# Kernel tuning notes

Measured on AMD Instinct MI355X. Metric: run time of the kernel, lower is better.

Reference implementation:

```python
import jax, jax.numpy as jnp
import numpy as np

NU, NI, NB, D = 100000, 50000, 20000, 64
E_UI, E_UB, E_BI = 1_000_000, 600_000, 400_000
BATCH = 2048
NUM_LAYERS = 2
C_TEMP = 0.25


def _sym_laplacian(src, dst, n_src_offset, n_total):
    # bipartite graph made symmetric: edges (u, off+v) and (off+v, u), val 1.0
    row = np.concatenate([src, n_src_offset + dst])
    col = np.concatenate([n_src_offset + dst, src])
    deg = np.bincount(row, minlength=n_total).astype(np.float64)
    val = 1.0 / ((np.sqrt(deg[row]) + 1e-8) * (np.sqrt(deg[col]) + 1e-8))
    return row.astype(np.int32), col.astype(np.int32), val.astype(np.float32)


def setup_inputs() -> dict:
    rng = np.random.default_rng(0)
    ui_u = rng.integers(0, NU, E_UI)
    ui_i = rng.integers(0, NI, E_UI)
    ub_u = rng.integers(0, NU, E_UB)
    ub_b = rng.integers(0, NB, E_UB)
    bi_b = rng.integers(0, NB, E_BI)
    bi_i = rng.integers(0, NI, E_BI)

    il_row, il_col, il_val = _sym_laplacian(ui_u, ui_i, NU, NU + NI)
    bl_row, bl_col, bl_val = _sym_laplacian(ub_u, ub_b, NU, NU + NB)
    deg_b = np.bincount(bi_b, minlength=NB).astype(np.float64)
    agg_val = (1.0 / (deg_b + 1e-8))[bi_b].astype(np.float32)

    key = jax.random.key(0)
    k1, k2, k3 = jax.random.split(key, 3)
    std = 0.05  # xavier-ish init scale
    return {
        "users_feature": jax.random.normal(k1, (NU, D), jnp.float32) * std,
        "items_feature": jax.random.normal(k2, (NI, D), jnp.float32) * std,
        "bundles_feature": jax.random.normal(k3, (NB, D), jnp.float32) * std,
        "il_row": jnp.asarray(il_row), "il_col": jnp.asarray(il_col), "il_val": jnp.asarray(il_val),
        "bl_row": jnp.asarray(bl_row), "bl_col": jnp.asarray(bl_col), "bl_val": jnp.asarray(bl_val),
        "agg_row": jnp.asarray(bi_b.astype(np.int32)), "agg_col": jnp.asarray(bi_i.astype(np.int32)),
        "agg_val": jnp.asarray(agg_val),
        "users": jnp.asarray(rng.integers(0, NU, BATCH).astype(np.int32)),
        "bundles": jnp.asarray(rng.integers(0, NB, (BATCH, 2)).astype(np.int32)),
    }


def _spmm(row, col, val, feat, n):
    # COO SpMM: out[r] += val * feat[c]   (gather + segment-sum, memory bound)
    return jax.ops.segment_sum(val[:, None] * feat[col], row, num_segments=n)


def _one_propagate(row, col, val, A, B):
    f = jnp.concatenate([A, B], axis=0)
    n = f.shape[0]
    acc = f
    for i in range(NUM_LAYERS):
        f = _spmm(row, col, val, f, n) / (i + 2)
        nrm = jnp.maximum(jnp.linalg.norm(f, axis=1, keepdims=True), 1e-12)
        acc = acc + f / nrm
    return acc[: A.shape[0]], acc[A.shape[0]:]


def _c_loss(pos, aug):
    pos = pos / jnp.maximum(jnp.linalg.norm(pos, axis=1, keepdims=True), 1e-12)
    aug = aug / jnp.maximum(jnp.linalg.norm(aug, axis=1, keepdims=True), 1e-12)
    pos_score = jnp.sum(pos * aug, axis=1) / C_TEMP
    ttl = (pos @ aug.T) / C_TEMP
    return -jnp.mean(pos_score - jax.scipy.special.logsumexp(ttl, axis=1))


def reference(users_feature, items_feature, bundles_feature,
              il_row, il_col, il_val, bl_row, bl_col, bl_val,
              agg_row, agg_col, agg_val, users, bundles):
    # item-level propagation over symmetric (U+I) graph
    IL_u, IL_i = _one_propagate(il_row, il_col, il_val, users_feature, items_feature)
    # bundle rep from item-level: row-normalized [B,I] spmm
    IL_b = _spmm(agg_row, agg_col, agg_val, IL_i, bundles_feature.shape[0])
    # bundle-level propagation over symmetric (U+B) graph
    BL_u, BL_b = _one_propagate(bl_row, bl_col, bl_val, users_feature, bundles_feature)

    # BPR on (pos, neg) bundle pairs, summing both views
    pred = (jnp.sum(IL_u[users][:, None, :] * IL_b[bundles], axis=-1)
            + jnp.sum(BL_u[users][:, None, :] * BL_b[bundles], axis=-1))  # [BATCH, 2]
    bpr_loss = jnp.mean(jax.nn.softplus(pred[:, 1] - pred[:, 0]))  # -log sigmoid(pos-neg)

    c_loss = 0.5 * (_c_loss(IL_u[users], BL_u[users]) + _c_loss(IL_b[bundles[:, 0]], BL_b[bundles[:, 0]]))
    return jnp.stack([bpr_loss, c_loss])
```

## Files before the change

### kernel.cpp

```cpp
#include <hip/hip_runtime.h>
#include <hip/hip_fp16.h>
#include <math.h>

#define DD 64
#define INV_TEMP 4.0f
#define MAXBINS 1280
#define BINSHIFT 8
#define CAP 10240
#define ECAP (CAP / 256)
#define COLBITS 18
#define K1 32.0f
#define K2_OVER_K1 4.0f

typedef float v2f __attribute__((ext_vector_type(2)));

__device__ __forceinline__ float waveSum(float x) {
#pragma unroll
    for (int off = 32; off > 0; off >>= 1) x += __shfl_xor(x, off, 64);
    return x;
}

__device__ __forceinline__ unsigned packH2(float a, float b) {
    __half2 h = __halves2half2(__float2half_rn(a), __float2half_rn(b));
    return *(unsigned*)&h;
}
__device__ __forceinline__ float2 unpackH2(unsigned u) {
    __half2 h = *(__half2*)&u;
    return __half22float2(h);
}
__device__ __forceinline__ unsigned packFp8x4(float a, float b, float c, float d) {
    int v = __builtin_amdgcn_cvt_pk_fp8_f32(a, b, 0, false);
    v = __builtin_amdgcn_cvt_pk_fp8_f32(c, d, v, true);
    return (unsigned)v;
}

__device__ __forceinline__ void accFp8(uint4 d,
    v2f& a0, v2f& a1, v2f& a2, v2f& a3,
    v2f& a4, v2f& a5, v2f& a6, v2f& a7)
{
    a0 += __builtin_amdgcn_cvt_pk_f32_fp8((int)d.x, false);
    a1 += __builtin_amdgcn_cvt_pk_f32_fp8((int)d.x, true);
    a2 += __builtin_amdgcn_cvt_pk_f32_fp8((int)d.y, false);
    a3 += __builtin_amdgcn_cvt_pk_f32_fp8((int)d.y, true);
    a4 += __builtin_amdgcn_cvt_pk_f32_fp8((int)d.z, false);
    a5 += __builtin_amdgcn_cvt_pk_f32_fp8((int)d.z, true);
    a6 += __builtin_amdgcn_cvt_pk_f32_fp8((int)d.w, false);
    a7 += __builtin_amdgcn_cvt_pk_f32_fp8((int)d.w, true);
}

__device__ __forceinline__ void accH16(uint4 d,
    v2f& a0, v2f& a1, v2f& a2, v2f& a3)
{
    float2 h0 = unpackH2(d.x), h1 = unpackH2(d.y);
    float2 h2 = unpackH2(d.z), h3 = unpackH2(d.w);
    a0[0] += h0.x; a0[1] += h0.y; a1[0] += h1.x; a1[1] += h1.y;
    a2[0] += h2.x; a2[1] += h2.y; a3[0] += h3.x; a3[1] += h3.y;
}


__device__ __forceinline__ int fetchRow(
    int i, const int* __restrict__ r1, const int* __restrict__ r2,
    const int* __restrict__ r3, int E1, int E12, int b2, int b3)
{
    if (i < E1)  return __builtin_nontemporal_load(&r1[i]);
    if (i < E12) return b2 + __builtin_nontemporal_load(&r2[i - E1]);
    return b3 + __builtin_nontemporal_load(&r3[i - E12]);
}

__device__ __forceinline__ void fetchEdge(
    int i, const int* __restrict__ r1, const int* __restrict__ c1,
    const int* __restrict__ r2, const int* __restrict__ c2,
    const int* __restrict__ r3, const int* __restrict__ c3,
    int E1, int E12, int b2, int b3, int& row, int& col)
{
    if (i < E1)       { row = __builtin_nontemporal_load(&r1[i]);
                        col = __builtin_nontemporal_load(&c1[i]); }
    else if (i < E12) { int j = i - E1;
                        row = b2 + __builtin_nontemporal_load(&r2[j]);
                        col = __builtin_nontemporal_load(&c2[j]); }
    else              { int j = i - E12;
                        row = b3 + __builtin_nontemporal_load(&r3[j]);
                        col = __builtin_nontemporal_load(&c3[j]); }
}

__global__ void __launch_bounds__(1024)
binA_kernel(
    const int* __restrict__ r1, const int* __restrict__ c1,
    const int* __restrict__ r2, const int* __restrict__ c2,
    const int* __restrict__ r3, const int* __restrict__ c3,
    int E1, int E2, int E3, int b2, int b3, int nbins,
    int* __restrict__ binCursor, unsigned* __restrict__ binned,
    int chunk, int Etot)
{
    __shared__ int hist[MAXBINS];
    __shared__ int resv[MAXBINS];
    __shared__ int cur[MAXBINS];
    int t = threadIdx.x;
    for (int b = t; b < nbins; b += 1024) hist[b] = 0;
    __syncthreads();
    int lo = blockIdx.x * chunk;
    int hi = min(lo + chunk, Etot);
    int E12 = E1 + E2;
    for (int i = lo + t; i < hi; i += 1024) {
        int row = fetchRow(i, r1, r2, r3, E1, E12, b2, b3);
        atomicAdd(&hist[row >> BINSHIFT], 1);
    }
    __syncthreads();
    for (int b = t; b < nbins; b += 1024) {
        int h = hist[b];
        resv[b] = h ? atomicAdd(&binCursor[b], h) : 0;
        cur[b] = 0;
    }
    __syncthreads();
    for (int i = lo + t; i < hi; i += 1024) {
        int row, col;
        fetchEdge(i, r1, c1, r2, c2, r3, c3, E1, E12, b2, b3, row, col);
        int b = row >> BINSHIFT;
        int off = atomicAdd(&cur[b], 1);
        unsigned v = ((unsigned)(row & 255) << COLBITS) | (unsigned)col;
        binned[(size_t)b * CAP + resv[b] + off] = v;
    }
}

__global__ void __launch_bounds__(256) binB_kernel(
    unsigned* __restrict__ binned, const int* __restrict__ binCursor,
    int ntot,
    int* __restrict__ cnt, int* __restrict__ rowStart)
{
    __shared__ int hist[256];
    __shared__ int wtot[4];
    int b = blockIdx.x;
    size_t base = (size_t)b * CAP;
    int len = min(binCursor[b], CAP);
    int rowLo = b << BINSHIFT;
    int t = threadIdx.x;
    hist[t] = 0;
    __syncthreads();

    unsigned ent[ECAP];
#pragma unroll
    for (int k = 0; k < ECAP; k++) {
        int i = t + (k << 8);
        if (i < len) {
            unsigned u = __builtin_nontemporal_load(&binned[base + i]);
            ent[k] = u;
            atomicAdd(&hist[u >> COLBITS], 1);
        }
    }
    __syncthreads();

    int v = hist[t];
    int lane = t & 63, w = t >> 6;
    int sc = v;
    for (int off = 1; off < 64; off <<= 1) {
        int u = __shfl_up(sc, off, 64);
        if (lane >= off) sc += u;
    }
    if (lane == 63) wtot[w] = sc;
    __syncthreads();
    int woff = 0;
    for (int i = 0; i < w; i++) woff += wtot[i];
    int ex = woff + sc - v;
    hist[t] = ex;
    int grow = rowLo + t;
    if (grow < ntot) { cnt[grow] = v; rowStart[grow] = (int)base + ex; }
    __syncthreads();

#pragma unroll
    for (int k = 0; k < ECAP; k++) {
        int i = t + (k << 8);
        if (i < len) {
            unsigned u = ent[k];
            int p = atomicAdd(&hist[u >> COLBITS], 1);
            binned[base + p] = u & ((1u << COLBITS) - 1);
        }
    }
}

__global__ void __launch_bounds__(256) prep_kernel(
    const float* __restrict__ usersF, const float* __restrict__ itemsF,
    const float* __restrict__ bundF, const int* __restrict__ cnt,
    int NUv, int NIv, int NBv, int n1,
    unsigned* __restrict__ g01, unsigned* __restrict__ g02)
{
    int total = (NUv + NIv + NBv) * 16;
    int stride = gridDim.x * blockDim.x;
    for (int idx = blockIdx.x * blockDim.x + threadIdx.x; idx < total; idx += stride) {
        int rl = idx >> 4, pr = idx & 15;
        if (rl < NUv) {
            float4 f = *((const float4*)(usersF + (size_t)rl * DD) + pr);
            float s1 = K1 / (sqrtf((float)cnt[rl]) + 1e-8f);
            float s2 = K1 / (sqrtf((float)cnt[n1 + rl]) + 1e-8f);
            g01[(size_t)rl * 16 + pr] = packFp8x4(f.x*s1, f.y*s1, f.z*s1, f.w*s1);
            g02[(size_t)rl * 16 + pr] = packFp8x4(f.x*s2, f.y*s2, f.z*s2, f.w*s2);
        } else if (rl < NUv + NIv) {
            int r = rl - NUv;
            float4 f = *((const float4*)(itemsF + (size_t)r * DD) + pr);
            float s = K1 / (sqrtf((float)cnt[NUv + r]) + 1e-8f);
            g01[(size_t)(NUv + r) * 16 + pr] = packFp8x4(f.x*s, f.y*s, f.z*s, f.w*s);
        } else {
            int r = rl - NUv - NIv;
            float4 f = *((const float4*)(bundF + (size_t)r * DD) + pr);
            float s = K1 / (sqrtf((float)cnt[n1 + NUv + r]) + 1e-8f);
            g02[(size_t)(NUv + r) * 16 + pr] = packFp8x4(f.x*s, f.y*s, f.z*s, f.w*s);
        }
    }
}

__global__ void __launch_bounds__(256) spmm_l1(
    const int* __restrict__ rowStart, const int* __restrict__ cnt,
    const int* __restrict__ cs, int n1, int nAll,
    const unsigned* __restrict__ g01, const unsigned* __restrict__ g02,
    unsigned* __restrict__ g11, unsigned* __restrict__ g12,
    __half* __restrict__ nrm11, __half* __restrict__ nrm12)
{
    int lane = threadIdx.x & 63;
    int grp  = lane >> 2;
    int sub  = lane & 3;
    int wave = (blockIdx.x * blockDim.x + threadIdx.x) >> 6;
    int nW   = (gridDim.x * blockDim.x) >> 6;
    for (int g0 = wave * 16; g0 < nAll; g0 += nW * 16) {
        int g = g0 + grp;
        bool valid = g < nAll;
        int gi = valid ? g : nAll - 1;
        int start = rowStart[gi];
        int deg   = valid ? cnt[gi] : 0;
        bool first = gi < n1;
        const unsigned* tab = first ? g01 : g02;
        const int* csp = cs + start;
        v2f a0 = {0.f,0.f}, a1 = {0.f,0.f}, a2 = {0.f,0.f}, a3 = {0.f,0.f};
        v2f a4 = {0.f,0.f}, a5 = {0.f,0.f}, a6 = {0.f,0.f}, a7 = {0.f,0.f};
        int k = 0;
        for (; k + 4 <= deg; k += 4) {
            int c0 = csp[k], c1 = csp[k + 1], c2 = csp[k + 2], c3 = csp[k + 3];
            uint4 d0 = *((const uint4*)(tab + (size_t)c0 * 16) + sub);
            uint4 d1 = *((const uint4*)(tab + (size_t)c1 * 16) + sub);
            uint4 d2 = *((const uint4*)(tab + (size_t)c2 * 16) + sub);
            uint4 d3 = *((const uint4*)(tab + (size_t)c3 * 16) + sub);
            accFp8(d0, a0, a1, a2, a3, a4, a5, a6, a7);
            accFp8(d1, a0, a1, a2, a3, a4, a5, a6, a7);
            accFp8(d2, a0, a1, a2, a3, a4, a5, a6, a7);
            accFp8(d3, a0, a1, a2, a3, a4, a5, a6, a7);
        }
        for (; k < deg; k++) {
            int c = csp[k];
            uint4 d = *((const uint4*)(tab + (size_t)c * 16) + sub);
            accFp8(d, a0, a1, a2, a3, a4, a5, a6, a7);
        }
        float ns = a0[0]*a0[0] + a0[1]*a0[1] + a1[0]*a1[0] + a1[1]*a1[1]
                 + a2[0]*a2[0] + a2[1]*a2[1] + a3[0]*a3[0] + a3[1]*a3[1]
                 + a4[0]*a4[0] + a4[1]*a4[1] + a5[0]*a5[0] + a5[1]*a5[1]
                 + a6[0]*a6[0] + a6[1]*a6[1] + a7[0]*a7[0] + a7[1]*a7[1];
        ns += __shfl_xor(ns, 1, 64);
        ns += __shfl_xor(ns, 2, 64);
        float inv = 1.0f / fmaxf(sqrtf(ns), 1e-12f);
        float s = 1.0f / (sqrtf((float)deg) + 1e-8f);
        float m = K2_OVER_K1 * s * s;
        if (valid) {
            unsigned* o8p = first ? g11 + (size_t)g * 16
                                  : g12 + (size_t)(g - n1) * 16;
            __half* o16p = first ? nrm11 + (size_t)g * DD
                                 : nrm12 + (size_t)(g - n1) * DD;
            uint4 o8;
            o8.x = packFp8x4(a0[0]*m, a0[1]*m, a1[0]*m, a1[1]*m);
            o8.y = packFp8x4(a2[0]*m, a2[1]*m, a3[0]*m, a3[1]*m);
            o8.z = packFp8x4(a4[0]*m, a4[1]*m, a5[0]*m, a5[1]*m);
            o8.w = packFp8x4(a6[0]*m, a6[1]*m, a7[0]*m, a7[1]*m);
            *((uint4*)o8p + sub) = o8;
            uint4 oA, oB;
            oA.x = packH2(a0[0]*inv, a0[1]*inv);
            oA.y = packH2(a1[0]*inv, a1[1]*inv);
            oA.z = packH2(a2[0]*inv, a2[1]*inv);
            oA.w = packH2(a3[0]*inv, a3[1]*inv);
            oB.x = packH2(a4[0]*inv, a4[1]*inv);
            oB.y = packH2(a5[0]*inv, a5[1]*inv);
            oB.z = packH2(a6[0]*inv, a6[1]*inv);
            oB.w = packH2(a7[0]*inv, a7[1]*inv);
            *((uint4*)o16p + sub * 2)     = oA;
            *((uint4*)o16p + sub * 2 + 1) = oB;
        }
    }
}

__global__ void __launch_bounds__(256) spmm_l2(
    const int* __restrict__ rowStart, const int* __restrict__ cnt,
    const int* __restrict__ cs, int n1, int nAll, int NUv,
    const unsigned* __restrict__ g11, const unsigned* __restrict__ g12,
    const float* __restrict__ usersF, const float* __restrict__ itemsF,
    const float* __restrict__ bundF,
    const __half* __restrict__ nrm11, const __half* __restrict__ nrm12,
    __half* __restrict__ accIL, __half* __restrict__ accBL)
{
    int lane = threadIdx.x & 63;
    int grp  = lane >> 2;
    int sub  = lane & 3;
    int wave = (blockIdx.x * blockDim.x + threadIdx.x) >> 6;
    int nW   = (gridDim.x * blockDim.x) >> 6;
    for (int g0 = wave * 16; g0 < nAll; g0 += nW * 16) {
        int g = g0 + grp;
        bool valid = g < nAll;
        int gi = valid ? g : nAll - 1;
        int start = rowStart[gi];
        int deg   = valid ? cnt[gi] : 0;
        bool first = gi < n1;
        const unsigned* tab = first ? g11 : g12;
        const int* csp = cs + start;
        v2f a0 = {0.f,0.f}, a1 = {0.f,0.f}, a2 = {0.f,0.f}, a3 = {0.f,0.f};
        v2f a4 = {0.f,0.f}, a5 = {0.f,0.f}, a6 = {0.f,0.f}, a7 = {0.f,0.f};
        int k = 0;
        for (; k + 4 <= deg; k += 4) {
            int c0 = csp[k], c1 = csp[k + 1], c2 = csp[k + 2], c3 = csp[k + 3];
            uint4 d0 = *((const uint4*)(tab + (size_t)c0 * 16) + sub);
            uint4 d1 = *((const uint4*)(tab + (size_t)c1 * 16) + sub);
            uint4 d2 = *((const uint4*)(tab + (size_t)c2 * 16) + sub);
            uint4 d3 = *((const uint4*)(tab + (size_t)c3 * 16) + sub);
            accFp8(d0, a0, a1, a2, a3, a4, a5, a6, a7);
            accFp8(d1, a0, a1, a2, a3, a4, a5, a6, a7);
            accFp8(d2, a0, a1, a2, a3, a4, a5, a6, a7);
            accFp8(d3, a0, a1, a2, a3, a4, a5, a6, a7);
        }
        for (; k < deg; k++) {
            int c = csp[k];
            uint4 d = *((const uint4*)(tab + (size_t)c * 16) + sub);
            accFp8(d, a0, a1, a2, a3, a4, a5, a6, a7);
        }
        float ns = a0[0]*a0[0] + a0[1]*a0[1] + a1[0]*a1[0] + a1[1]*a1[1]
                 + a2[0]*a2[0] + a2[1]*a2[1] + a3[0]*a3[0] + a3[1]*a3[1]
                 + a4[0]*a4[0] + a4[1]*a4[1] + a5[0]*a5[0] + a5[1]*a5[1]
                 + a6[0]*a6[0] + a6[1]*a6[1] + a7[0]*a7[0] + a7[1]*a7[1];
        ns += __shfl_xor(ns, 1, 64);
        ns += __shfl_xor(ns, 2, 64);
        float inv = 1.0f / fmaxf(sqrtf(ns), 1e-12f);
        if (valid) {
            int r = first ? g : g - n1;
            const float* f0base =
                first ? ((r < NUv) ? usersF + (size_t)r * DD
                                   : itemsF + (size_t)(r - NUv) * DD)
                      : ((r < NUv) ? usersF + (size_t)r * DD
                                   : bundF + (size_t)(r - NUv) * DD);
            const __half* nrmIn = first ? nrm11 + (size_t)g * DD
                                        : nrm12 + (size_t)r * DD;
            __half* outp = first ? accIL + (size_t)g * DD
                                 : accBL + (size_t)r * DD;
            float4 f0 = *((const float4*)f0base + sub * 4);
            float4 f1 = *((const float4*)f0base + sub * 4 + 1);
            float4 f2 = *((const float4*)f0base + sub * 4 + 2);
            float4 f3 = *((const float4*)f0base + sub * 4 + 3);
            uint4 nvA = *((const uint4*)nrmIn + sub * 2);
            uint4 nvB = *((const uint4*)nrmIn + sub * 2 + 1);
            float2 m0 = unpackH2(nvA.x), m1 = unpackH2(nvA.y);
            float2 m2 = unpackH2(nvA.z), m3 = unpackH2(nvA.w);
            float2 m4 = unpackH2(nvB.x), m5 = unpackH2(nvB.y);
            float2 m6 = unpackH2(nvB.z), m7 = unpackH2(nvB.w);
            uint4 oA, oB;
            oA.x = packH2(f0.x + m0.x + a0[0]*inv, f0.y + m0.y + a0[1]*inv);
            oA.y = packH2(f0.z + m1.x + a1[0]*inv, f0.w + m1.y + a1[1]*inv);
            oA.z = packH2(f1.x + m2.x + a2[0]*inv, f1.y + m2.y + a2[1]*inv);
            oA.w = packH2(f1.z + m3.x + a3[0]*inv, f1.w + m3.y + a3[1]*inv);
            oB.x = packH2(f2.x + m4.x + a4[0]*inv, f2.y + m4.y + a4[1]*inv);
            oB.y = packH2(f2.z + m5.x + a5[0]*inv, f2.w + m5.y + a5[1]*inv);
            oB.z = packH2(f3.x + m6.x + a6[0]*inv, f3.y + m6.y + a6[1]*inv);
            oB.w = packH2(f3.z + m7.x + a7[0]*inv, f3.w + m7.y + a7[1]*inv);
            *((uint4*)outp + sub * 2)     = oA;
            *((uint4*)outp + sub * 2 + 1) = oB;
        }
    }
}

__global__ void __launch_bounds__(256) spmm_agg(
    const int* __restrict__ rowStart, const int* __restrict__ cnt,
    const int* __restrict__ cs, int rbase,
    const __half* __restrict__ table16, __half* __restrict__ out16, int n)
{
    int lane = threadIdx.x & 63;
    int grp  = lane >> 3;
    int sub  = lane & 7;
    int wave = (blockIdx.x * blockDim.x + threadIdx.x) >> 6;
    int nW   = (gridDim.x * blockDim.x) >> 6;
    for (int r0 = wave * 8; r0 < n; r0 += nW * 8) {
        int r = r0 + grp;
        bool valid = r < n;
        int idx = rbase + (valid ? r : n - 1);
        int start = rowStart[idx];
        int deg   = valid ? cnt[idx] : 0;
        const int* csp = cs + start;
        v2f a0 = {0.f, 0.f}, a1 = {0.f, 0.f}, a2 = {0.f, 0.f}, a3 = {0.f, 0.f};
        int k = 0;
        for (; k + 4 <= deg; k += 4) {
            int c0 = csp[k], c1 = csp[k + 1], c2 = csp[k + 2], c3 = csp[k + 3];
            uint4 d0 = *((const uint4*)(table16 + (size_t)c0 * DD) + sub);
            uint4 d1 = *((const uint4*)(table16 + (size_t)c1 * DD) + sub);
            uint4 d2 = *((const uint4*)(table16 + (size_t)c2 * DD) + sub);
            uint4 d3 = *((const uint4*)(table16 + (size_t)c3 * DD) + sub);
            accH16(d0, a0, a1, a2, a3);
            accH16(d1, a0, a1, a2, a3);
            accH16(d2, a0, a1, a2, a3);
            accH16(d3, a0, a1, a2, a3);
        }
        for (; k < deg; k++) {
            int c = csp[k];
            uint4 d = *((const uint4*)(table16 + (size_t)c * DD) + sub);
            accH16(d, a0, a1, a2, a3);
        }
        float sc2 = 1.0f / ((float)deg + 1e-8f);
        if (valid) {
            uint4 o;
            o.x = packH2(a0[0]*sc2, a0[1]*sc2);
            o.y = packH2(a1[0]*sc2, a1[1]*sc2);
            o.z = packH2(a2[0]*sc2, a2[1]*sc2);
            o.w = packH2(a3[0]*sc2, a3[1]*sc2);
            *((uint4*)(out16 + (size_t)r * DD) + sub) = o;
        }
    }
}


__global__ void batch_kernel(
    const int* __restrict__ users, const int* __restrict__ bundles,
    const __half* __restrict__ IL, const __half* __restrict__ ILb,
    const __half* __restrict__ BL, int NUv,
    float* __restrict__ pos1, float* __restrict__ aug1,
    float* __restrict__ pos2, float* __restrict__ aug2,
    float* __restrict__ sums, int batch)
{
    int lane = threadIdx.x & 63;
    int wave = (blockIdx.x * blockDim.x + threadIdx.x) >> 6;
    int nW   = (gridDim.x * blockDim.x) >> 6;
    for (int b = wave; b < batch; b += nW) {
        int u   = users[b];
        int bp  = bundles[2 * b];
        int bn  = bundles[2 * b + 1];
        float ilu  = __half2float(IL [(size_t)u * DD + lane]);
        float blu  = __half2float(BL [(size_t)u * DD + lane]);
        float ilb0 = __half2float(ILb[(size_t)bp * DD + lane]);
        float ilb1 = __half2float(ILb[(size_t)bn * DD + lane]);
        float blb0 = __half2float(BL [(size_t)(NUv + bp) * DD + lane]);
        float blb1 = __half2float(BL [(size_t)(NUv + bn) * DD + lane]);
        float d0 = waveSum(ilu * ilb0 + blu * blb0);
        float d1 = waveSum(ilu * ilb1 + blu * blb1);
        float x  = d1 - d0;
        float sp = fmaxf(x, 0.f) + log1pf(expf(-fabsf(x)));
        if (lane == 0) atomicAdd(&sums[0], sp);
        float nilu = sqrtf(waveSum(ilu * ilu));
        float nblu = sqrtf(waveSum(blu * blu));
        float nilb = sqrtf(waveSum(ilb0 * ilb0));
        float nblb = sqrtf(waveSum(blb0 * blb0));
        pos1[(size_t)b * DD + lane] = ilu  / fmaxf(nilu, 1e-12f);
        aug1[(size_t)b * DD + lane] = blu  / fmaxf(nblu, 1e-12f);
        pos2[(size_t)b * DD + lane] = ilb0 / fmaxf(nilb, 1e-12f);
        aug2[(size_t)b * DD + lane] = blb0 / fmaxf(nblb, 1e-12f);
    }
}

__device__ __forceinline__ void load_tile_T(const float* __restrict__ src, int rowBase,
                                            int batch, float* __restrict__ dst, int tx) {
    int i = tx >> 2, c = tx & 3;
#pragma unroll
    for (int t = 0; t < 4; t++) {
        int k0 = c * 4 + t * 16;
        float4 v = make_float4(0.f, 0.f, 0.f, 0.f);
        int gi = rowBase + i;
        if (gi < batch) v = *(const float4*)&src[(size_t)gi * DD + k0];
        dst[(k0 + 0) * 68 + i] = v.x;
        dst[(k0 + 1) * 68 + i] = v.y;
        dst[(k0 + 2) * 68 + i] = v.z;
        dst[(k0 + 3) * 68 + i] = v.w;
    }
}

__global__ void closs_kernel(
    const float* __restrict__ pos1, const float* __restrict__ aug1,
    const float* __restrict__ pos2, const float* __restrict__ aug2,
    float* __restrict__ S, float* __restrict__ Dg, int batch, int jChunk)
{
    const float* pos = blockIdx.z ? pos2 : pos1;
    const float* aug = blockIdx.z ? aug2 : aug1;
    __shared__ float Pt[64 * 68];
    __shared__ float At[64 * 68];
    __shared__ float red[64 * 17];
    int tx = threadIdx.x;
    int iBase = blockIdx.x * 64;
    int jBeg = blockIdx.y * jChunk;
    int jEnd = min(jBeg + jChunk, batch);
    load_tile_T(pos, iBase, batch, Pt, tx);
    int tr = tx >> 4, tc = tx & 15;
    float rs[4] = {0.f, 0.f, 0.f, 0.f};
    for (int j0 = jBeg; j0 < jEnd; j0 += 64) {
        __syncthreads();
        load_tile_T(aug, j0, batch, At, tx);
        __syncthreads();
        float acc[16];
#pragma unroll
        for (int q = 0; q < 16; q++) acc[q] = 0.f;
#pragma unroll 8
        for (int k = 0; k < 64; k++) {
            float4 pv = *(const float4*)&Pt[k * 68 + 4 * tr];
            float4 av = *(const float4*)&At[k * 68 + 4 * tc];
            acc[0]  += pv.x * av.x;  acc[1]  += pv.x * av.y;
            acc[2]  += pv.x * av.z;  acc[3]  += pv.x * av.w;
            acc[4]  += pv.y * av.x;  acc[5]  += pv.y * av.y;
            acc[6]  += pv.y * av.z;  acc[7]  += pv.y * av.w;
            acc[8]  += pv.z * av.x;  acc[9]  += pv.z * av.y;
            acc[10] += pv.z * av.z;  acc[11] += pv.z * av.w;
            acc[12] += pv.w * av.x;  acc[13] += pv.w * av.y;
            acc[14] += pv.w * av.z;  acc[15] += pv.w * av.w;
        }
#pragma unroll
        for (int qi = 0; qi < 4; qi++) {
            int gi = iBase + 4 * tr + qi;
#pragma unroll
            for (int qj = 0; qj < 4; qj++) {
                int gj = j0 + 4 * tc + qj;
                float t = acc[qi * 4 + qj] * INV_TEMP;
                if (gi < batch && gj < batch) {
                    rs[qi] += __expf(t);
                    if (gi == gj) Dg[blockIdx.z * batch + gi] = t;
                }
            }
        }
    }
    __syncthreads();
#pragma unroll
    for (int qi = 0; qi < 4; qi++) red[(4 * tr + qi) * 17 + tc] = rs[qi];
    __syncthreads();
    if (tx < 64) {
        float s = 0.f;
#pragma unroll
        for (int c = 0; c < 16; c++) s += red[tx * 17 + c];
        int gi = iBase + tx;
        if (gi < batch) atomicAdd(&S[blockIdx.z * batch + gi], s);
    }
}

__global__ void closs_finish(const float* __restrict__ S, const float* __restrict__ Dg,
                             const float* __restrict__ sums,
                             float* __restrict__ out, int batch, float invB)
{
    int tid = threadIdx.x;
    __shared__ float wsm[2][4];
    float tot[2];
#pragma unroll
    for (int m = 0; m < 2; m++) {
        float local = 0.f;
        for (int i = tid; i < batch; i += blockDim.x)
            local += logf(S[m * batch + i]) - Dg[m * batch + i];
        local = waveSum(local);
        if ((tid & 63) == 0) wsm[m][tid >> 6] = local;
    }
    __syncthreads();
    if (tid == 0) {
#pragma unroll
        for (int m = 0; m < 2; m++)
            tot[m] = wsm[m][0] + wsm[m][1] + wsm[m][2] + wsm[m][3];
        out[0] = sums[0] * invB;
        out[1] = 0.5f * (tot[0] + tot[1]) * invB;
    }
}


extern "C" void kernel_launch(void* const* d_in, const int* in_sizes, int n_in,
                              void* d_out, int out_size, void* d_ws, size_t ws_size,
                              hipStream_t stream)
{
    const float* usersF = (const float*)d_in[0];
    const float* itemsF = (const float*)d_in[1];
    const float* bundF  = (const float*)d_in[2];
    const int*   il_row = (const int*)d_in[3];
    const int*   il_col = (const int*)d_in[4];
    const int*   bl_row = (const int*)d_in[6];
    const int*   bl_col = (const int*)d_in[7];
    const int*   agg_row = (const int*)d_in[9];
    const int*   agg_col = (const int*)d_in[10];
    const int*   users   = (const int*)d_in[12];
    const int*   bundles = (const int*)d_in[13];

    const int NUv = in_sizes[0] / DD;
    const int NIv = in_sizes[1] / DD;
    const int NBv = in_sizes[2] / DD;
    const int E1 = in_sizes[3], E2 = in_sizes[6], E3 = in_sizes[9];
    const int batch = in_sizes[12];
    const int n1 = NUv + NIv;
    const int n2 = NUv + NBv;
    const int ntot = n1 + n2 + NBv;
    const int Etot = E1 + E2 + E3;
    const int nbins = (ntot + 255) >> BINSHIFT;

    float* ws = (float*)d_ws;
    size_t off = 0;
    float* sums = ws + off;      off += 16;
    float* S    = ws + off;      off += (size_t)2 * batch;
    float* Dg   = ws + off;      off += (size_t)2 * batch;
    float* pos1 = ws + off;      off += (size_t)batch * DD;
    float* aug1 = ws + off;      off += (size_t)batch * DD;
    float* pos2 = ws + off;      off += (size_t)batch * DD;
    float* aug2 = ws + off;      off += (size_t)batch * DD;
    int*   cnt  = (int*)(ws + off);      off += (size_t)ntot;
    int*   rowStart = (int*)(ws + off);  off += (size_t)ntot;
    int*   binCursor = (int*)(ws + off); off += MAXBINS;
    off = (off + 3) & ~(size_t)3;
    unsigned* binned = (unsigned*)(ws + off); off += (size_t)nbins * CAP;
    unsigned* g01 = (unsigned*)(ws + off); off += (size_t)n1 * 16;
    unsigned* g11 = (unsigned*)(ws + off); off += (size_t)n1 * 16;
    unsigned* g02 = (unsigned*)(ws + off); off += (size_t)n2 * 16;
    unsigned* g12 = (unsigned*)(ws + off); off += (size_t)n2 * 16;
    off = (off + 3) & ~(size_t)3;
    __half* hbase = (__half*)(ws + off);
    size_t hoff = 0;
    __half* nrm11 = hbase + hoff;  hoff += (size_t)n1 * DD;
    __half* accIL = hbase + hoff;  hoff += (size_t)n1 * DD;
    __half* nrm12 = hbase + hoff;  hoff += (size_t)n2 * DD;
    __half* accBL = hbase + hoff;  hoff += (size_t)n2 * DD;
    __half* ILb   = hbase + hoff;  hoff += (size_t)NBv * DD;
    (void)ws_size;

    hipMemsetAsync(sums, 0, 16 * sizeof(float), stream);
    hipMemsetAsync(S, 0, (size_t)2 * batch * sizeof(float), stream);
    hipMemsetAsync(binCursor, 0, MAXBINS * sizeof(int), stream);

    const int nA = 256;
    int chunk = (Etot + nA - 1) / nA;
    binA_kernel<<<nA, 1024, 0, stream>>>(
        il_row, il_col, bl_row, bl_col, agg_row, agg_col,
        E1, E2, E3, n1, n1 + n2, nbins, binCursor, binned, chunk, Etot);
    binB_kernel<<<nbins, 256, 0, stream>>>(
        binned, binCursor, ntot, cnt, rowStart);

    prep_kernel<<<2048, 256, 0, stream>>>(
        usersF, itemsF, bundF, cnt, NUv, NIv, NBv, n1, g01, g02);

    const int* cs = (const int*)binned;
    const int nAll = n1 + n2;

    auto grid16 = [](int n) { return (n + 63) / 64; };
    auto grid8  = [](int n) { return (n + 31) / 32; };

    spmm_l1<<<grid16(nAll), 256, 0, stream>>>(
        rowStart, cnt, cs, n1, nAll, g01, g02, g11, g12, nrm11, nrm12);

    spmm_l2<<<grid16(nAll), 256, 0, stream>>>(
        rowStart, cnt, cs, n1, nAll, NUv, g11, g12,
        usersF, itemsF, bundF, nrm11, nrm12, accIL, accBL);

    spmm_agg<<<grid8(NBv), 256, 0, stream>>>(
        rowStart, cnt, cs, n1 + n2, accIL + (size_t)NUv * DD, ILb, NBv);

    batch_kernel<<<(batch + 3) / 4, 256, 0, stream>>>(
        users, bundles, accIL, ILb, accBL, NUv,
        pos1, aug1, pos2, aug2, sums, batch);

    const int yChunks = 8;
    int jChunk = ((batch + yChunks * 64 - 1) / (yChunks * 64)) * 64;
    dim3 cg2((batch + 63) / 64, yChunks, 2);
    closs_kernel<<<cg2, 256, 0, stream>>>(pos1, aug1, pos2, aug2, S, Dg, batch, jChunk);
    closs_finish<<<1, 256, 0, stream>>>(S, Dg, sums, (float*)d_out, batch,
                                        1.0f / (float)batch);
}
```

Baseline: 384.6 us.

## Use fp16 feature copy, nontemporal loads/stores, 512-thread binB, padded SpMM tails

Several independent changes. prep_kernel now writes an fp16 copy of the raw features, and spmm_l2 reads that copy instead of the fp32 originals to cut residual-add traffic. Edge-index loads and the output stores in the SpMM kernels switch to nontemporal hints. The scalar tail loops are replaced by one three-wide padded step. binB now runs 512 threads per bin with fewer entries per thread. In exchange there is an extra write pass in prep and fp16 rounding of the base features added to the layer sums.

```diff
diff --git a/kernel.cpp b/kernel.cpp
--- a/kernel.cpp
+++ b/kernel.cpp
@@ -7,12 +7,27 @@
 #define MAXBINS 1280
 #define BINSHIFT 8
 #define CAP 10240
-#define ECAP (CAP / 256)
+#define ECAP2 (CAP / 512)
 #define COLBITS 18
 #define K1 32.0f
 #define K2_OVER_K1 4.0f
 
 typedef float v2f __attribute__((ext_vector_type(2)));
+typedef unsigned u32x4 __attribute__((ext_vector_type(4)));
+typedef unsigned u32x2 __attribute__((ext_vector_type(2)));
+
+__device__ __forceinline__ uint4 ntload4(const void* p) {
+    u32x4 v = __builtin_nontemporal_load((const u32x4*)p);
+    uint4 r; r.x = v.x; r.y = v.y; r.z = v.z; r.w = v.w; return r;
+}
+__device__ __forceinline__ void ntstore4(uint4 d, void* p) {
+    u32x4 v; v.x = d.x; v.y = d.y; v.z = d.z; v.w = d.w;
+    __builtin_nontemporal_store(v, (u32x4*)p);
+}
+__device__ __forceinline__ void ntstore2(uint2 d, void* p) {
+    u32x2 v; v.x = d.x; v.y = d.y;
+    __builtin_nontemporal_store(v, (u32x2*)p);
+}
 
 __device__ __forceinline__ float waveSum(float x) {
 #pragma unroll
@@ -57,6 +72,8 @@
     a2[0] += h2.x; a2[1] += h2.y; a3[0] += h3.x; a3[1] += h3.y;
 }
 
+__device__ __forceinline__ void zero4(uint4& d) { d.x = 0; d.y = 0; d.z = 0; d.w = 0; }
+
 
 __device__ __forceinline__ int fetchRow(
     int i, const int* __restrict__ r1, const int* __restrict__ r2,
@@ -122,7 +139,7 @@
     }
 }
 
-__global__ void __launch_bounds__(256) binB_kernel(
+__global__ void __launch_bounds__(512) binB_kernel(
     unsigned* __restrict__ binned, const int* __restrict__ binCursor,
     int ntot,
     int* __restrict__ cnt, int* __restrict__ rowStart)
@@ -134,13 +151,13 @@
     int len = min(binCursor[b], CAP);
     int rowLo = b << BINSHIFT;
     int t = threadIdx.x;
-    hist[t] = 0;
-    __syncthreads();
-
-    unsigned ent[ECAP];
-#pragma unroll
-    for (int k = 0; k < ECAP; k++) {
-        int i = t + (k << 8);
+    if (t < 256) hist[t] = 0;
+    __syncthreads();
+
+    unsigned ent[ECAP2];
+#pragma unroll
+    for (int k = 0; k < ECAP2; k++) {
+        int i = t + (k << 9);
         if (i < len) {
             unsigned u = __builtin_nontemporal_load(&binned[base + i]);
             ent[k] = u;
@@ -149,26 +166,30 @@
     }
     __syncthreads();
 
-    int v = hist[t];
+    int v = 0, sc = 0, grow = rowLo + t;
     int lane = t & 63, w = t >> 6;
-    int sc = v;
-    for (int off = 1; off < 64; off <<= 1) {
-        int u = __shfl_up(sc, off, 64);
-        if (lane >= off) sc += u;
-    }
-    if (lane == 63) wtot[w] = sc;
-    __syncthreads();
-    int woff = 0;
-    for (int i = 0; i < w; i++) woff += wtot[i];
-    int ex = woff + sc - v;
-    hist[t] = ex;
-    int grow = rowLo + t;
-    if (grow < ntot) { cnt[grow] = v; rowStart[grow] = (int)base + ex; }
-    __syncthreads();
-
-#pragma unroll
-    for (int k = 0; k < ECAP; k++) {
-        int i = t + (k << 8);
+    if (t < 256) {
+        v = hist[t];
+        sc = v;
+        for (int off = 1; off < 64; off <<= 1) {
+            int u = __shfl_up(sc, off, 64);
+            if (lane >= off) sc += u;
+        }
+        if (lane == 63) wtot[w] = sc;
+    }
+    __syncthreads();
+    if (t < 256) {
+        int woff = 0;
+        for (int i = 0; i < w; i++) woff += wtot[i];
+        int ex = woff + sc - v;
+        hist[t] = ex;
+        if (grow < ntot) { cnt[grow] = v; rowStart[grow] = (int)base + ex; }
+    }
+    __syncthreads();
+
+#pragma unroll
+    for (int k = 0; k < ECAP2; k++) {
+        int i = t + (k << 9);
         if (i < len) {
             unsigned u = ent[k];
             int p = atomicAdd(&hist[u >> COLBITS], 1);
@@ -181,29 +202,35 @@
     const float* __restrict__ usersF, const float* __restrict__ itemsF,
     const float* __restrict__ bundF, const int* __restrict__ cnt,
     int NUv, int NIv, int NBv, int n1,
-    unsigned* __restrict__ g01, unsigned* __restrict__ g02)
+    unsigned* __restrict__ g01, unsigned* __restrict__ g02,
+    unsigned* __restrict__ hfeat)
 {
     int total = (NUv + NIv + NBv) * 16;
     int stride = gridDim.x * blockDim.x;
     for (int idx = blockIdx.x * blockDim.x + threadIdx.x; idx < total; idx += stride) {
         int rl = idx >> 4, pr = idx & 15;
+        float4 f;
         if (rl < NUv) {
-            float4 f = *((const float4*)(usersF + (size_t)rl * DD) + pr);
+            f = *((const float4*)(usersF + (size_t)rl * DD) + pr);
             float s1 = K1 / (sqrtf((float)cnt[rl]) + 1e-8f);
             float s2 = K1 / (sqrtf((float)cnt[n1 + rl]) + 1e-8f);
             g01[(size_t)rl * 16 + pr] = packFp8x4(f.x*s1, f.y*s1, f.z*s1, f.w*s1);
             g02[(size_t)rl * 16 + pr] = packFp8x4(f.x*s2, f.y*s2, f.z*s2, f.w*s2);
         } else if (rl < NUv + NIv) {
             int r = rl - NUv;
-            float4 f = *((const float4*)(itemsF + (size_t)r * DD) + pr);
+            f = *((const float4*)(itemsF + (size_t)r * DD) + pr);
             float s = K1 / (sqrtf((float)cnt[NUv + r]) + 1e-8f);
             g01[(size_t)(NUv + r) * 16 + pr] = packFp8x4(f.x*s, f.y*s, f.z*s, f.w*s);
         } else {
             int r = rl - NUv - NIv;
-            float4 f = *((const float4*)(bundF + (size_t)r * DD) + pr);
+            f = *((const float4*)(bundF + (size_t)r * DD) + pr);
             float s = K1 / (sqrtf((float)cnt[n1 + NUv + r]) + 1e-8f);
             g02[(size_t)(NUv + r) * 16 + pr] = packFp8x4(f.x*s, f.y*s, f.z*s, f.w*s);
         }
+        uint2 h;
+        h.x = packH2(f.x, f.y);
+        h.y = packH2(f.z, f.w);
+        ntstore2(h, hfeat + (size_t)rl * 32 + pr * 2);
     }
 }
 
@@ -232,7 +259,10 @@
         v2f a4 = {0.f,0.f}, a5 = {0.f,0.f}, a6 = {0.f,0.f}, a7 = {0.f,0.f};
         int k = 0;
         for (; k + 4 <= deg; k += 4) {
-            int c0 = csp[k], c1 = csp[k + 1], c2 = csp[k + 2], c3 = csp[k + 3];
+            int c0 = __builtin_nontemporal_load(&csp[k]);
+            int c1 = __builtin_nontemporal_load(&csp[k + 1]);
+            int c2 = __builtin_nontemporal_load(&csp[k + 2]);
+            int c3 = __builtin_nontemporal_load(&csp[k + 3]);
             uint4 d0 = *((const uint4*)(tab + (size_t)c0 * 16) + sub);
             uint4 d1 = *((const uint4*)(tab + (size_t)c1 * 16) + sub);
             uint4 d2 = *((const uint4*)(tab + (size_t)c2 * 16) + sub);
@@ -242,10 +272,18 @@
             accFp8(d2, a0, a1, a2, a3, a4, a5, a6, a7);
             accFp8(d3, a0, a1, a2, a3, a4, a5, a6, a7);
         }
-        for (; k < deg; k++) {
-            int c = csp[k];
-            uint4 d = *((const uint4*)(tab + (size_t)c * 16) + sub);
-            accFp8(d, a0, a1, a2, a3, a4, a5, a6, a7);
+        if (k < deg) {
+            int c0 = __builtin_nontemporal_load(&csp[k]);
+            int c1 = (k + 1 < deg) ? __builtin_nontemporal_load(&csp[k + 1]) : 0;
+            int c2 = (k + 2 < deg) ? __builtin_nontemporal_load(&csp[k + 2]) : 0;
+            uint4 d0 = *((const uint4*)(tab + (size_t)c0 * 16) + sub);
+            uint4 d1 = *((const uint4*)(tab + (size_t)c1 * 16) + sub);
+            uint4 d2 = *((const uint4*)(tab + (size_t)c2 * 16) + sub);
+            if (k + 1 >= deg) zero4(d1);
+            if (k + 2 >= deg) zero4(d2);
+            accFp8(d0, a0, a1, a2, a3, a4, a5, a6, a7);
+            accFp8(d1, a0, a1, a2, a3, a4, a5, a6, a7);
+            accFp8(d2, a0, a1, a2, a3, a4, a5, a6, a7);
         }
         float ns = a0[0]*a0[0] + a0[1]*a0[1] + a1[0]*a1[0] + a1[1]*a1[1]
                  + a2[0]*a2[0] + a2[1]*a2[1] + a3[0]*a3[0] + a3[1]*a3[1]
@@ -257,16 +295,17 @@
         float s = 1.0f / (sqrtf((float)deg) + 1e-8f);
         float m = K2_OVER_K1 * s * s;
         if (valid) {
-            unsigned* o8p = first ? g11 + (size_t)g * 16
-                                  : g12 + (size_t)(g - n1) * 16;
-            __half* o16p = first ? nrm11 + (size_t)g * DD
-                                 : nrm12 + (size_t)(g - n1) * DD;
+            int r = first ? g : g - n1;
+            unsigned* o8p = first ? g11 + (size_t)r * 16
+                                  : g12 + (size_t)r * 16;
+            __half* o16p = first ? nrm11 + (size_t)r * DD
+                                 : nrm12 + (size_t)r * DD;
             uint4 o8;
             o8.x = packFp8x4(a0[0]*m, a0[1]*m, a1[0]*m, a1[1]*m);
             o8.y = packFp8x4(a2[0]*m, a2[1]*m, a3[0]*m, a3[1]*m);
             o8.z = packFp8x4(a4[0]*m, a4[1]*m, a5[0]*m, a5[1]*m);
             o8.w = packFp8x4(a6[0]*m, a6[1]*m, a7[0]*m, a7[1]*m);
-            *((uint4*)o8p + sub) = o8;
+            ntstore4(o8, (uint4*)o8p + sub);
             uint4 oA, oB;
             oA.x = packH2(a0[0]*inv, a0[1]*inv);
             oA.y = packH2(a1[0]*inv, a1[1]*inv);
@@ -276,8 +315,8 @@
             oB.y = packH2(a5[0]*inv, a5[1]*inv);
             oB.z = packH2(a6[0]*inv, a6[1]*inv);
             oB.w = packH2(a7[0]*inv, a7[1]*inv);
-            *((uint4*)o16p + sub * 2)     = oA;
-            *((uint4*)o16p + sub * 2 + 1) = oB;
+            ntstore4(oA, (uint4*)o16p + sub * 2);
+            ntstore4(oB, (uint4*)o16p + sub * 2 + 1);
         }
     }
 }
@@ -286,8 +325,7 @@
     const int* __restrict__ rowStart, const int* __restrict__ cnt,
     const int* __restrict__ cs, int n1, int nAll, int NUv,
     const unsigned* __restrict__ g11, const unsigned* __restrict__ g12,
-    const float* __restrict__ usersF, const float* __restrict__ itemsF,
-    const float* __restrict__ bundF,
+    const unsigned* __restrict__ hfeat,
     const __half* __restrict__ nrm11, const __half* __restrict__ nrm12,
     __half* __restrict__ accIL, __half* __restrict__ accBL)
 {
@@ -309,7 +347,10 @@
         v2f a4 = {0.f,0.f}, a5 = {0.f,0.f}, a6 = {0.f,0.f}, a7 = {0.f,0.f};
         int k = 0;
         for (; k + 4 <= deg; k += 4) {
-            int c0 = csp[k], c1 = csp[k + 1], c2 = csp[k + 2], c3 = csp[k + 3];
+            int c0 = __builtin_nontemporal_load(&csp[k]);
+            int c1 = __builtin_nontemporal_load(&csp[k + 1]);
+            int c2 = __builtin_nontemporal_load(&csp[k + 2]);
+            int c3 = __builtin_nontemporal_load(&csp[k + 3]);
             uint4 d0 = *((const uint4*)(tab + (size_t)c0 * 16) + sub);
             uint4 d1 = *((const uint4*)(tab + (size_t)c1 * 16) + sub);
             uint4 d2 = *((const uint4*)(tab + (size_t)c2 * 16) + sub);
@@ -319,10 +360,18 @@
             accFp8(d2, a0, a1, a2, a3, a4, a5, a6, a7);
             accFp8(d3, a0, a1, a2, a3, a4, a5, a6, a7);
         }
-        for (; k < deg; k++) {
-            int c = csp[k];
-            uint4 d = *((const uint4*)(tab + (size_t)c * 16) + sub);
-            accFp8(d, a0, a1, a2, a3, a4, a5, a6, a7);
+        if (k < deg) {
+            int c0 = __builtin_nontemporal_load(&csp[k]);
+            int c1 = (k + 1 < deg) ? __builtin_nontemporal_load(&csp[k + 1]) : 0;
+            int c2 = (k + 2 < deg) ? __builtin_nontemporal_load(&csp[k + 2]) : 0;
+            uint4 d0 = *((const uint4*)(tab + (size_t)c0 * 16) + sub);
+            uint4 d1 = *((const uint4*)(tab + (size_t)c1 * 16) + sub);
+            uint4 d2 = *((const uint4*)(tab + (size_t)c2 * 16) + sub);
+            if (k + 1 >= deg) zero4(d1);
+            if (k + 2 >= deg) zero4(d2);
+            accFp8(d0, a0, a1, a2, a3, a4, a5, a6, a7);
+            accFp8(d1, a0, a1, a2, a3, a4, a5, a6, a7);
+            accFp8(d2, a0, a1, a2, a3, a4, a5, a6, a7);
         }
         float ns = a0[0]*a0[0] + a0[1]*a0[1] + a1[0]*a1[0] + a1[1]*a1[1]
                  + a2[0]*a2[0] + a2[1]*a2[1] + a3[0]*a3[0] + a3[1]*a3[1]
@@ -333,36 +382,37 @@
         float inv = 1.0f / fmaxf(sqrtf(ns), 1e-12f);
         if (valid) {
             int r = first ? g : g - n1;
-            const float* f0base =
-                first ? ((r < NUv) ? usersF + (size_t)r * DD
-                                   : itemsF + (size_t)(r - NUv) * DD)
-                      : ((r < NUv) ? usersF + (size_t)r * DD
-                                   : bundF + (size_t)(r - NUv) * DD);
-            const __half* nrmIn = first ? nrm11 + (size_t)g * DD
+            const unsigned* hf =
+                first ? hfeat + (size_t)g * 32
+                      : ((r < NUv) ? hfeat + (size_t)r * 32
+                                   : hfeat + (size_t)(n1 + (r - NUv)) * 32);
+            const __half* nrmIn = first ? nrm11 + (size_t)r * DD
                                         : nrm12 + (size_t)r * DD;
-            __half* outp = first ? accIL + (size_t)g * DD
+            __half* outp = first ? accIL + (size_t)r * DD
                                  : accBL + (size_t)r * DD;
-            float4 f0 = *((const float4*)f0base + sub * 4);
-            float4 f1 = *((const float4*)f0base + sub * 4 + 1);
-            float4 f2 = *((const float4*)f0base + sub * 4 + 2);
-            float4 f3 = *((const float4*)f0base + sub * 4 + 3);
-            uint4 nvA = *((const uint4*)nrmIn + sub * 2);
-            uint4 nvB = *((const uint4*)nrmIn + sub * 2 + 1);
+            uint4 fA = ntload4((const uint4*)hf + sub * 2);
+            uint4 fB = ntload4((const uint4*)hf + sub * 2 + 1);
+            float2 f0 = unpackH2(fA.x), f1 = unpackH2(fA.y);
+            float2 f2 = unpackH2(fA.z), f3 = unpackH2(fA.w);
+            float2 f4 = unpackH2(fB.x), f5 = unpackH2(fB.y);
+            float2 f6 = unpackH2(fB.z), f7 = unpackH2(fB.w);
+            uint4 nvA = ntload4((const uint4*)nrmIn + sub * 2);
+            uint4 nvB = ntload4((const uint4*)nrmIn + sub * 2 + 1);
             float2 m0 = unpackH2(nvA.x), m1 = unpackH2(nvA.y);
             float2 m2 = unpackH2(nvA.z), m3 = unpackH2(nvA.w);
             float2 m4 = unpackH2(nvB.x), m5 = unpackH2(nvB.y);
             float2 m6 = unpackH2(nvB.z), m7 = unpackH2(nvB.w);
             uint4 oA, oB;
             oA.x = packH2(f0.x + m0.x + a0[0]*inv, f0.y + m0.y + a0[1]*inv);
-            oA.y = packH2(f0.z + m1.x + a1[0]*inv, f0.w + m1.y + a1[1]*inv);
-            oA.z = packH2(f1.x + m2.x + a2[0]*inv, f1.y + m2.y + a2[1]*inv);
-            oA.w = packH2(f1.z + m3.x + a3[0]*inv, f1.w + m3.y + a3[1]*inv);
-            oB.x = packH2(f2.x + m4.x + a4[0]*inv, f2.y + m4.y + a4[1]*inv);
-            oB.y = packH2(f2.z + m5.x + a5[0]*inv, f2.w + m5.y + a5[1]*inv);
-            oB.z = packH2(f3.x + m6.x + a6[0]*inv, f3.y + m6.y + a6[1]*inv);
-            oB.w = packH2(f3.z + m7.x + a7[0]*inv, f3.w + m7.y + a7[1]*inv);
-            *((uint4*)outp + sub * 2)     = oA;
-            *((uint4*)outp + sub * 2 + 1) = oB;
+            oA.y = packH2(f1.x + m1.x + a1[0]*inv, f1.y + m1.y + a1[1]*inv);
+            oA.z = packH2(f2.x + m2.x + a2[0]*inv, f2.y + m2.y + a2[1]*inv);
+            oA.w = packH2(f3.x + m3.x + a3[0]*inv, f3.y + m3.y + a3[1]*inv);
+            oB.x = packH2(f4.x + m4.x + a4[0]*inv, f4.y + m4.y + a4[1]*inv);
+            oB.y = packH2(f5.x + m5.x + a5[0]*inv, f5.y + m5.y + a5[1]*inv);
+            oB.z = packH2(f6.x + m6.x + a6[0]*inv, f6.y + m6.y + a6[1]*inv);
+            oB.w = packH2(f7.x + m7.x + a7[0]*inv, f7.y + m7.y + a7[1]*inv);
+            ntstore4(oA, (uint4*)outp + sub * 2);
+            ntstore4(oB, (uint4*)outp + sub * 2 + 1);
         }
     }
 }
@@ -387,7 +437,10 @@
         v2f a0 = {0.f, 0.f}, a1 = {0.f, 0.f}, a2 = {0.f, 0.f}, a3 = {0.f, 0.f};
         int k = 0;
         for (; k + 4 <= deg; k += 4) {
-            int c0 = csp[k], c1 = csp[k + 1], c2 = csp[k + 2], c3 = csp[k + 3];
+            int c0 = __builtin_nontemporal_load(&csp[k]);
+            int c1 = __builtin_nontemporal_load(&csp[k + 1]);
+            int c2 = __builtin_nontemporal_load(&csp[k + 2]);
+            int c3 = __builtin_nontemporal_load(&csp[k + 3]);
             uint4 d0 = *((const uint4*)(table16 + (size_t)c0 * DD) + sub);
             uint4 d1 = *((const uint4*)(table16 + (size_t)c1 * DD) + sub);
             uint4 d2 = *((const uint4*)(table16 + (size_t)c2 * DD) + sub);
@@ -397,10 +450,18 @@
             accH16(d2, a0, a1, a2, a3);
             accH16(d3, a0, a1, a2, a3);
         }
-        for (; k < deg; k++) {
-            int c = csp[k];
-            uint4 d = *((const uint4*)(table16 + (size_t)c * DD) + sub);
-            accH16(d, a0, a1, a2, a3);
+        if (k < deg) {
+            int c0 = __builtin_nontemporal_load(&csp[k]);
+            int c1 = (k + 1 < deg) ? __builtin_nontemporal_load(&csp[k + 1]) : 0;
+            int c2 = (k + 2 < deg) ? __builtin_nontemporal_load(&csp[k + 2]) : 0;
+            uint4 d0 = *((const uint4*)(table16 + (size_t)c0 * DD) + sub);
+            uint4 d1 = *((const uint4*)(table16 + (size_t)c1 * DD) + sub);
+            uint4 d2 = *((const uint4*)(table16 + (size_t)c2 * DD) + sub);
+            if (k + 1 >= deg) zero4(d1);
+            if (k + 2 >= deg) zero4(d2);
+            accH16(d0, a0, a1, a2, a3);
+            accH16(d1, a0, a1, a2, a3);
+            accH16(d2, a0, a1, a2, a3);
         }
         float sc2 = 1.0f / ((float)deg + 1e-8f);
         if (valid) {
@@ -409,7 +470,7 @@
             o.y = packH2(a1[0]*sc2, a1[1]*sc2);
             o.z = packH2(a2[0]*sc2, a2[1]*sc2);
             o.w = packH2(a3[0]*sc2, a3[1]*sc2);
-            *((uint4*)(out16 + (size_t)r * DD) + sub) = o;
+            ntstore4(o, (uint4*)(out16 + (size_t)r * DD) + sub);
         }
     }
 }
@@ -603,6 +664,7 @@
     unsigned* g11 = (unsigned*)(ws + off); off += (size_t)n1 * 16;
     unsigned* g02 = (unsigned*)(ws + off); off += (size_t)n2 * 16;
     unsigned* g12 = (unsigned*)(ws + off); off += (size_t)n2 * 16;
+    unsigned* hfeat = (unsigned*)(ws + off); off += (size_t)(n1 + NBv) * 32;
     off = (off + 3) & ~(size_t)3;
     __half* hbase = (__half*)(ws + off);
     size_t hoff = 0;
@@ -622,11 +684,11 @@
     binA_kernel<<<nA, 1024, 0, stream>>>(
         il_row, il_col, bl_row, bl_col, agg_row, agg_col,
         E1, E2, E3, n1, n1 + n2, nbins, binCursor, binned, chunk, Etot);
-    binB_kernel<<<nbins, 256, 0, stream>>>(
+    binB_kernel<<<nbins, 512, 0, stream>>>(
         binned, binCursor, ntot, cnt, rowStart);
 
     prep_kernel<<<2048, 256, 0, stream>>>(
-        usersF, itemsF, bundF, cnt, NUv, NIv, NBv, n1, g01, g02);
+        usersF, itemsF, bundF, cnt, NUv, NIv, NBv, n1, g01, g02, hfeat);
 
     const int* cs = (const int*)binned;
     const int nAll = n1 + n2;
@@ -639,7 +701,7 @@
 
     spmm_l2<<<grid16(nAll), 256, 0, stream>>>(
         rowStart, cnt, cs, n1, nAll, NUv, g11, g12,
-        usersF, itemsF, bundF, nrm11, nrm12, accIL, accBL);
+        hfeat, nrm11, nrm12, accIL, accBL);
 
     spmm_agg<<<grid8(NBv), 256, 0, stream>>>(
         rowStart, cnt, cs, n1 + n2, accIL + (size_t)NUv * DD, ILb, NBv);
```

Measured after the change: 399.1 us. +3.8%, slower.
